# Kernel optimization log

Hardware: AMD Instinct MI355X
Metric: run time of the kernel (lower is better)

Reference implementation:

```python
import jax, jax.numpy as jnp
import numpy as np

EMB_DIM = 32
UID_TGT = 200000
IID_TGT = 50000
BATCH = 128
TOPK = 50000          # hardcoded inside test_source_free branch
TARGET_LABEL = 4.0    # module-level target rating constant


def setup_inputs() -> dict:
    key = jax.random.key(0)
    k1, k2, k3, k4, k5 = jax.random.split(key, 5)
    # x: column 0 = item id (stored as float, like the torch code), cols 1: = src_rate_pre
    iid = jax.random.randint(k1, (BATCH,), 0, IID_TGT).astype(jnp.float32)
    src_rate = jax.random.normal(k2, (BATCH, EMB_DIM), dtype=jnp.float32)
    x = jnp.concatenate([iid[:, None], src_rate], axis=1)  # [B, 1+D]
    uid_weight = 0.1 * jax.random.normal(k3, (UID_TGT, EMB_DIM), dtype=jnp.float32)
    iid_weight = 0.1 * jax.random.normal(k4, (IID_TGT, EMB_DIM), dtype=jnp.float32)
    rp_weight = 0.1 * jax.random.normal(k5, (EMB_DIM, EMB_DIM), dtype=jnp.float32)
    return {"x": x, "uid_weight": uid_weight, "iid_weight": iid_weight, "rp_weight": rp_weight}


def reference(x, uid_weight, iid_weight, rp_weight):
    # === stage == 'test_source_free' ===
    iid = x[:, 0].astype(jnp.int32)                     # [B]
    iid_emb = iid_weight[iid]                           # [B, D] item embedding gather
    src_rate_pre = x[:, 1:] @ rp_weight.T               # [B, D] Linear(emb,emb,bias=False)
    # |uid_emb . src_rate - target|  (torch: [U,B]; here kept [B,U])
    predict_rate = jnp.abs(src_rate_pre @ uid_weight.T - TARGET_LABEL)  # [B, U]
    # torch: full sort ascending + take first TOPK  ==  bottom-TOPK per row
    _, topk_idx = jax.lax.top_k(-predict_rate, TOPK)    # [B, TOPK]
    # voted rating = <selected user emb, item emb>; compute all dots once,
    # then gather (same math as gathering [B,TOPK,D] embeddings and dotting).
    all_scores = iid_emb @ uid_weight.T                 # [B, U]
    voted_rating = jnp.take_along_axis(all_scores, topk_idx, axis=1)  # [B, TOPK]
    mean_rating = jnp.mean(voted_rating, axis=1)        # [B]
    return mean_rating
```

## Files before the change

kernel.cpp:

```cpp
#include <hip/hip_runtime.h>
#include <hip/hip_bf16.h>
#include <stdint.h>

#define EMB    32
#define BATCH  128
#define NU     200000
#define KSEL   50000
#define XCOLS  33
#define SLOTS  32
#define G1     512
#define G2P    512
#define G2F    256
#define HISTW  (128 * 129)
#define T1     32
#define T2     64

#define OFF_SPRE   0
#define OFF_IIDE   16384
#define OFF_GHIST  32768
#define OFF_BASE16 163840
#define OFF_PREFIX 164352
#define OFF_M2     164864
#define OFF_EQ     165376
#define OFF_CAND   173568
#define OFF_PART   173568
#define PART_BYTES ((size_t)G1 * HISTW * 4)

__device__ __forceinline__ float xor1(float x) {
    int r = __builtin_amdgcn_update_dpp(0, __float_as_int(x), 0xB1, 0xF, 0xF, true);
    return __int_as_float(r);
}

__device__ __forceinline__ float dotrow(const float* __restrict__ c,
                                        const float* __restrict__ u) {
    float d = 0.f;
    #pragma unroll
    for (int q = 0; q < 8; ++q) {
        const float4 v = *(const float4*)(u + q * 4);
        d += c[4*q+0]*v.x + c[4*q+1]*v.y + c[4*q+2]*v.z + c[4*q+3]*v.w;
    }
    return d;
}

__global__ void prep_kernel(const float* __restrict__ x,
                            const float* __restrict__ iid_w,
                            const float* __restrict__ rp,
                            const float* __restrict__ uid,
                            float* __restrict__ s_pre,
                            float* __restrict__ iid_emb,
                            uint32_t* __restrict__ base16,
                            uint32_t* __restrict__ eq_cnt) {
    const int b = blockIdx.x;
    const int t = threadIdx.x;
    __shared__ float xr[EMB];
    if (t < EMB) xr[t] = x[b * XCOLS + 1 + t];
    if (t == 63) eq_cnt[b * 16] = 0u;
    __syncthreads();
    if (t < EMB) {
        float acc = 0.f;
        #pragma unroll
        for (int k = 0; k < EMB; ++k) acc += xr[k] * rp[t * EMB + k];
        s_pre[b * EMB + t] = acc;
    } else {
        const int d = t - EMB;
        const int iid = (int)x[b * XCOLS];
        iid_emb[b * EMB + d] = iid_w[(size_t)iid * EMB + d];
    }
    __syncthreads();
    if (t == 0) {
        float dot = 0.f;
        #pragma unroll
        for (int k = 0; k < EMB; ++k) dot += s_pre[b * EMB + k] * uid[k];
        const uint32_t bits = __float_as_uint(fabsf(dot - 4.0f));
        const uint32_t hi = bits >> 16;
        base16[b] = (hi > 128u) ? (hi - 128u) : 0u;
    }
}

__global__ void zero_kernel(uint32_t* __restrict__ p, int n) {
    int i = blockIdx.x * blockDim.x + threadIdx.x;
    if (i < n) p[i] = 0u;
}

template <bool PART>
__global__ __launch_bounds__(1024)
void sweep1_kernel(const float* __restrict__ s_pre,
                   const float* __restrict__ uid,
                   const uint32_t* __restrict__ base16,
                   uint32_t* __restrict__ gout,
                   int jchunk) {
    extern __shared__ uint32_t smem1[];
    uint32_t* hist = smem1;
    float* tiles = (float*)(smem1 + HISTW);
    const int t  = threadIdx.x;
    const int b  = t & 127;
    const int jl = t >> 7;
    for (int i = t; i < HISTW; i += 1024) hist[i] = 0u;
    float s[EMB];
    #pragma unroll
    for (int d = 0; d < EMB; ++d) s[d] = s_pre[b * EMB + d];
    const uint32_t base = base16[b];

    const int j0 = blockIdx.x * jchunk;
    const int jend = min(j0 + jchunk, NU);
    const int nt = (jend - j0 + T1 - 1) / T1;
    const int srow = t >> 5;

    {
        float v = 0.f;
        if (j0 + srow < NU) v = uid[(size_t)j0 * EMB + t];
        tiles[t] = v;
    }
    __syncthreads();

    for (int tt = 0; tt < nt; ++tt) {
        const int jt = j0 + tt * T1;
        const bool has_next = (tt + 1 < nt);
        float vnext = 0.f;
        if (has_next) {
            const int jn = jt + T1;
            if (jn + srow < NU) vnext = uid[(size_t)jn * EMB + t];
        }
        const float* tp = tiles + (tt & 1) * (T1 * EMB);
        const int lim = min(T1, jend - jt);
        for (int r = jl; r < lim; r += 8) {
            const float d0 = dotrow(s, tp + r * EMB);
            const uint32_t bits0 = __float_as_uint(fabsf(d0 - 4.0f));
            int dg0 = (int)(bits0 >> 16) - (int)base;
            dg0 = dg0 < 0 ? 0 : (dg0 > 255 ? 255 : dg0);
            atomicAdd(&hist[b * 129 + (dg0 >> 1)], 1u << ((dg0 & 1) * 16));
        }
        if (has_next) {
            tiles[((tt + 1) & 1) * (T1 * EMB) + t] = vnext;
        }
        __syncthreads();
    }
    if (PART) {
        uint32_t* part = gout + (size_t)blockIdx.x * HISTW;
        for (int i = t; i < HISTW; i += 1024) part[i] = hist[i];
    } else {
        for (int i = t; i < 128 * 256; i += 1024) {
            const int r = i >> 8, d = i & 255;
            const uint32_t c = (hist[r * 129 + (d >> 1)] >> ((d & 1) * 16)) & 0xFFFFu;
            if (c) atomicAdd(&gout[i], c);
        }
    }
}

__global__ void scan1_kernel(const uint32_t* __restrict__ ghist,
                             const uint32_t* __restrict__ base16,
                             uint32_t* __restrict__ prefix16,
                             uint32_t* __restrict__ m2) {
    const int b = threadIdx.x;
    uint32_t cum = 0, before = 0;
    int c1 = 255;
    for (int d = 0; d < 256; ++d) {
        const uint32_t c = ghist[b * 256 + d];
        if (cum + c >= (uint32_t)KSEL) { c1 = d; before = cum; break; }
        cum += c;
        if (d == 255) before = cum;
    }
    prefix16[b] = base16[b] + (uint32_t)c1;
    m2[b] = (uint32_t)KSEL - before;
}

__global__ __launch_bounds__(256)
void scan1_part_kernel(const uint32_t* __restrict__ part,
                       const uint32_t* __restrict__ base16,
                       uint32_t* __restrict__ prefix16,
                       uint32_t* __restrict__ m2) {
    const int row = blockIdx.x;
    const int t = threadIdx.x;
    __shared__ uint32_t h[256];
    const int sh = (t & 1) * 16;
    const uint32_t* p = part + (size_t)row * 129 + (t >> 1);
    uint32_t a0 = 0, a1 = 0, a2 = 0, a3 = 0;
    for (int g = 0; g < G1; g += 4) {
        a0 += (p[(size_t)(g + 0) * HISTW] >> sh) & 0xFFFFu;
        a1 += (p[(size_t)(g + 1) * HISTW] >> sh) & 0xFFFFu;
        a2 += (p[(size_t)(g + 2) * HISTW] >> sh) & 0xFFFFu;
        a3 += (p[(size_t)(g + 3) * HISTW] >> sh) & 0xFFFFu;
    }
    h[t] = a0 + a1 + a2 + a3;
    __syncthreads();
    if (t == 0) {
        uint32_t cum = 0, before = 0; int c1 = 255;
        for (int d = 0; d < 256; ++d) {
            const uint32_t c = h[d];
            if (cum + c >= (uint32_t)KSEL) { c1 = d; before = cum; break; }
            cum += c;
            if (d == 255) before = cum;
        }
        prefix16[row] = base16[row] + (uint32_t)c1;
        m2[row] = (uint32_t)KSEL - before;
    }
}

__global__ __launch_bounds__(1024)
void sweep2_kernel(const float* __restrict__ s_pre,
                   const float* __restrict__ iid_emb,
                   const float* __restrict__ uid,
                   const uint32_t* __restrict__ prefix16,
                   uint32_t* __restrict__ eq_cnt,
                   float* __restrict__ sum_part,
                   uint64_t* __restrict__ cand,
                   int cap, int jchunk) {
    extern __shared__ char smem2[];
    uint64_t* lcand  = (uint64_t*)smem2;
    float*    tiles  = (float*)(smem2 + 32768);
    uint32_t* lcnt   = (uint32_t*)(smem2 + 49152);
    uint32_t* lbase  = (uint32_t*)(smem2 + 49664);
    float*    sums_b = (float*)(smem2 + 50176);
    const int t   = threadIdx.x;
    const int par = t & 1;
    const int pr  = t >> 1;
    const int b   = pr & 127;
    const int jl  = pr >> 7;
    if (t < 128) { lcnt[t] = 0u; sums_b[t] = 0.f; }
    float c[EMB];
    {
        const float4* cp4 = (const float4*)((par ? iid_emb : s_pre) + b * EMB);
        #pragma unroll
        for (int q = 0; q < 8; ++q) {
            float4 v = cp4[q];
            c[4*q+0] = v.x; c[4*q+1] = v.y; c[4*q+2] = v.z; c[4*q+3] = v.w;
        }
    }
    const uint32_t pfx = prefix16[b];

    const int j0 = blockIdx.x * jchunk;
    const int jend = min(j0 + jchunk, NU);
    const int nt = (jend - j0 + T2 - 1) / T2;
    const int srow = t >> 4;

    {
        float2 v = make_float2(0.f, 0.f);
        if (j0 + srow < NU) v = *(const float2*)(uid + (size_t)j0 * EMB + t * 2);
        *(float2*)(tiles + t * 2) = v;
    }
    __syncthreads();

    float local = 0.f;
    for (int tt = 0; tt < nt; ++tt) {
        const int jt = j0 + tt * T2;
        const bool has_next = (tt + 1 < nt);
        float2 vnext = make_float2(0.f, 0.f);
        if (has_next) {
            const int jn = jt + T2;
            if (jn + srow < NU) vnext = *(const float2*)(uid + (size_t)jn * EMB + t * 2);
        }
        const float* tp = tiles + (tt & 1) * (T2 * EMB);
        const int lim = min(T2, jend - jt);
        for (int r = jl; r < lim; r += 4) {
            const float a0 = dotrow(c, tp + r * EMB);
            const float p0 = xor1(a0);
            if (par == 0) {
                const uint32_t bits0 = __float_as_uint(fabsf(a0 - 4.0f));
                const uint32_t hi0 = bits0 >> 16;
                local += (hi0 < pfx) ? p0 : 0.f;
                if (hi0 == pfx) {
                    const uint32_t pos = atomicAdd(&lcnt[b], 1u);
                    const uint64_t pk = ((uint64_t)bits0 << 32) | (uint32_t)(jt + r);
                    if (pos < (uint32_t)SLOTS) lcand[b * SLOTS + pos] = pk;
                    else {
                        const uint32_t g = atomicAdd(&eq_cnt[b * 16], 1u);
                        if (g < (uint32_t)cap) cand[(size_t)b * cap + g] = pk;
                    }
                }
            }
        }
        if (has_next) {
            *(float2*)(tiles + ((tt + 1) & 1) * (T2 * EMB) + t * 2) = vnext;
        }
        __syncthreads();
    }
    if (par == 0 && local != 0.f) atomicAdd(&sums_b[b], local);
    __syncthreads();
    if (t < 128) {
        sum_part[(size_t)blockIdx.x * 128 + t] = sums_b[t];
        const uint32_t n = min(lcnt[t], (uint32_t)SLOTS);
        lbase[t] = atomicAdd(&eq_cnt[t * 16], n);
    }
    __syncthreads();
    for (int i = t; i < 128 * SLOTS; i += 1024) {
        const int bb = i >> 5;
        const int sl = i & 31;
        if (sl < (int)min(lcnt[bb], (uint32_t)SLOTS)) {
            const uint32_t p = lbase[bb] + (uint32_t)sl;
            if (p < (uint32_t)cap) cand[(size_t)bb * cap + p] = lcand[i];
        }
    }
}

__global__ __launch_bounds__(256)
void final_kernel(const float* __restrict__ iid_emb,
                  const float* __restrict__ uid,
                  const uint32_t* __restrict__ m2_,
                  const uint32_t* __restrict__ eq_cnt,
                  const float* __restrict__ sum_part,
                  const uint64_t* __restrict__ cand,
                  int cap, int g2, float* __restrict__ out) {
    const int b = blockIdx.x;
    const int t = threadIdx.x;
    __shared__ float red[256];
    __shared__ uint32_t hist[256];
    __shared__ float e[EMB];
    __shared__ uint32_t tie[128];
    __shared__ uint32_t tiecnt, sc2, sm3, sc3, sm4;
    __shared__ float sbelow;
    if (t < EMB) e[t] = iid_emb[b * EMB + t];
    if (t == 0) tiecnt = 0u;
    hist[t] = 0u;
    {
        float acc = 0.f;
        for (int g = t; g < g2; g += 256) acc += sum_part[(size_t)g * 128 + b];
        red[t] = acc;
    }
    __syncthreads();
    for (int s = 128; s > 0; s >>= 1) { if (t < s) red[t] += red[t + s]; __syncthreads(); }
    if (t == 0) sbelow = red[0];
    __syncthreads();

    const uint32_t ec = eq_cnt[b * 16];
    const int cnt = (int)(ec < (uint32_t)cap ? ec : (uint32_t)cap);
    const uint64_t* cb = cand + (size_t)b * cap;

    for (int i = t; i < cnt; i += 256) {
        const uint32_t low16 = (uint32_t)(cb[i] >> 32) & 0xFFFFu;
        atomicAdd(&hist[low16 >> 8], 1u);
    }
    __syncthreads();
    if (t == 0) {
        const uint32_t m2v = m2_[b];
        uint32_t cum = 0, before = 0; int c2 = 255;
        for (int d = 0; d < 256; ++d) {
            const uint32_t c = hist[d];
            if (cum + c >= m2v) { c2 = d; before = cum; break; }
            cum += c;
        }
        sc2 = (uint32_t)c2; sm3 = m2v - before;
    }
    __syncthreads();
    const uint32_t c2 = sc2;
    hist[t] = 0u;
    __syncthreads();

    for (int i = t; i < cnt; i += 256) {
        const uint32_t low16 = (uint32_t)(cb[i] >> 32) & 0xFFFFu;
        if ((low16 >> 8) == c2) atomicAdd(&hist[low16 & 255u], 1u);
    }
    __syncthreads();
    if (t == 0) {
        const uint32_t m3 = sm3;
        uint32_t cum = 0, before = 0; int c3 = 255;
        for (int d = 0; d < 256; ++d) {
            const uint32_t c = hist[d];
            if (cum + c >= m3) { c3 = d; before = cum; break; }
            cum += c;
        }
        sc3 = (uint32_t)c3; sm4 = m3 - before;
    }
    __syncthreads();
    const uint32_t T16 = (c2 << 8) | sc3;

    float local = 0.f;
    for (int i = t; i < cnt; i += 256) {
        const uint64_t cv = cb[i];
        const uint32_t low16 = (uint32_t)(cv >> 32) & 0xFFFFu;
        if (low16 < T16) {
            const uint32_t j = (uint32_t)cv;
            const float4* u4 = (const float4*)(uid + (size_t)j * EMB);
            float dv = 0.f;
            #pragma unroll
            for (int q = 0; q < 8; ++q) {
                float4 u = u4[q];
                dv += e[4*q+0]*u.x + e[4*q+1]*u.y + e[4*q+2]*u.z + e[4*q+3]*u.w;
            }
            local += dv;
        } else if (low16 == T16) {
            const uint32_t pos = atomicAdd(&tiecnt, 1u);
            if (pos < 128u) tie[pos] = (uint32_t)cv;
        }
    }
    red[t] = local;
    __syncthreads();
    for (int s = 128; s > 0; s >>= 1) { if (t < s) red[t] += red[t + s]; __syncthreads(); }
    if (t == 0) {
        int tc = (int)(tiecnt < 128u ? tiecnt : 128u);
        for (int i = 1; i < tc; ++i) {
            const uint32_t v = tie[i]; int k = i - 1;
            while (k >= 0 && tie[k] > v) { tie[k+1] = tie[k]; --k; }
            tie[k+1] = v;
        }
        const int m4 = (int)sm4;
        float tsum = 0.f;
        for (int i = 0; i < m4 && i < tc; ++i) {
            const uint32_t j = tie[i];
            float dv = 0.f;
            for (int d = 0; d < EMB; ++d) dv += e[d] * uid[(size_t)j * EMB + d];
            tsum += dv;
        }
        out[b] = (sbelow + red[0] + tsum) / (float)KSEL;
    }
}

extern "C" void kernel_launch(void* const* d_in, const int* in_sizes, int n_in,
                              void* d_out, int out_size, void* d_ws, size_t ws_size,
                              hipStream_t stream) {
    const float* x     = (const float*)d_in[0];
    const float* uid   = (const float*)d_in[1];
    const float* iid_w = (const float*)d_in[2];
    const float* rp    = (const float*)d_in[3];
    float* out = (float*)d_out;

    char* ws = (char*)d_ws;
    float*    s_pre    = (float*)(ws + OFF_SPRE);
    float*    iid_emb  = (float*)(ws + OFF_IIDE);
    uint32_t* ghist    = (uint32_t*)(ws + OFF_GHIST);
    uint32_t* base16   = (uint32_t*)(ws + OFF_BASE16);
    uint32_t* prefix16 = (uint32_t*)(ws + OFF_PREFIX);
    uint32_t* m2       = (uint32_t*)(ws + OFF_M2);
    uint32_t* eq_cnt   = (uint32_t*)(ws + OFF_EQ);
    uint32_t* part     = (uint32_t*)(ws + OFF_PART);

    const size_t off_cand2 = OFF_PART + PART_BYTES;
    const bool use_part = ws_size >= off_cand2 + (size_t)128 * 8 * 4096;

    uint64_t* cand;
    int cap;
    float* sum_part;
    int g2;
    if (use_part) {
        cand = (uint64_t*)(ws + off_cand2);
        long long cap_ll = ((long long)ws_size - (long long)off_cand2) / (128LL * 8LL);
        cap = (int)(cap_ll > 16384 ? 16384 : cap_ll);
        sum_part = (float*)part;
        g2 = G2P;
    } else {
        cand = (uint64_t*)(ws + OFF_CAND);
        long long cap_ll = ((long long)ws_size - OFF_CAND) / (128LL * 8LL);
        cap = (int)(cap_ll > 16384 ? 16384 : (cap_ll < 1 ? 1 : cap_ll));
        sum_part = (float*)(ws + OFF_GHIST);
        g2 = G2F;
        const int n = (OFF_CAND - OFF_GHIST) / 4;
        zero_kernel<<<(n + 255) / 256, 256, 0, stream>>>((uint32_t*)(ws + OFF_GHIST), n);
    }

    prep_kernel<<<BATCH, 64, 0, stream>>>(x, iid_w, rp, uid, s_pre, iid_emb, base16, eq_cnt);

    const int jc1 = (NU + G1 - 1) / G1;
    const size_t lds1 = HISTW * 4 + 2 * T1 * EMB * 4;
    if (use_part) {
        sweep1_kernel<true><<<G1, 1024, lds1, stream>>>(s_pre, uid, base16, part, jc1);
        scan1_part_kernel<<<BATCH, 256, 0, stream>>>(part, base16, prefix16, m2);
    } else {
        sweep1_kernel<false><<<G1, 1024, lds1, stream>>>(s_pre, uid, base16, ghist, jc1);
        scan1_kernel<<<1, 128, 0, stream>>>(ghist, base16, prefix16, m2);
    }

    const int jc2 = (NU + g2 - 1) / g2;
    const size_t lds2 = 32768 + 16384 + 1536;
    sweep2_kernel<<<g2, 1024, lds2, stream>>>(s_pre, iid_emb, uid,
                                              prefix16, eq_cnt, sum_part,
                                              cand, cap, jc2);

    final_kernel<<<BATCH, 256, 0, stream>>>(iid_emb, uid, m2, eq_cnt, sum_part,
                                            cand, cap, g2, out);
}
```

Before: 225.3 us.

## Cache per-user high-16-bit digits in sweep1 to skip predict dot in sweep2

When the workspace is large enough, sweep1 now writes the high 16 bits of each |s·u-4| value to a [NU,128] uint16 buffer. A new sweep2 kernel reads these digits instead of recomputing the predict-rate dot product, so it computes only the item-score dot per user. Tie candidates store only the user index, and final_kernel recomputes their full bits. This trades about 51MB of extra global writes and reads against half of sweep2's arithmetic. The new path only runs if the workspace exceeds that size.

```diff
diff --git a/kernel.cpp b/kernel.cpp
--- a/kernel.cpp
+++ b/kernel.cpp
@@ -1,5 +1,4 @@
 #include <hip/hip_runtime.h>
-#include <hip/hip_bf16.h>
 #include <stdint.h>
 
 #define EMB    32
@@ -8,7 +7,9 @@
 #define KSEL   50000
 #define XCOLS  33
 #define SLOTS  32
+#define DSLOTS 16
 #define G1     512
+#define G2D    512
 #define G2P    512
 #define G2F    256
 #define HISTW  (128 * 129)
@@ -22,9 +23,11 @@
 #define OFF_PREFIX 164352
 #define OFF_M2     164864
 #define OFF_EQ     165376
-#define OFF_CAND   173568
-#define OFF_PART   173568
+#define OFF_BIG    173568
 #define PART_BYTES ((size_t)G1 * HISTW * 4)
+#define DIG_BYTES  ((size_t)NU * 128 * 2)
+#define OFF_PARTD  ((size_t)OFF_BIG + DIG_BYTES)
+#define OFF_CANDD  (OFF_PARTD + PART_BYTES)
 
 __device__ __forceinline__ float xor1(float x) {
     int r = __builtin_amdgcn_update_dpp(0, __float_as_int(x), 0xB1, 0xF, 0xF, true);
@@ -82,12 +85,13 @@
     if (i < n) p[i] = 0u;
 }
 
-template <bool PART>
+template <bool PART, bool DIG>
 __global__ __launch_bounds__(1024)
 void sweep1_kernel(const float* __restrict__ s_pre,
                    const float* __restrict__ uid,
                    const uint32_t* __restrict__ base16,
                    uint32_t* __restrict__ gout,
+                   uint16_t* __restrict__ dig,
                    int jchunk) {
     extern __shared__ uint32_t smem1[];
     uint32_t* hist = smem1;
@@ -126,7 +130,9 @@
         for (int r = jl; r < lim; r += 8) {
             const float d0 = dotrow(s, tp + r * EMB);
             const uint32_t bits0 = __float_as_uint(fabsf(d0 - 4.0f));
-            int dg0 = (int)(bits0 >> 16) - (int)base;
+            const uint32_t hi = bits0 >> 16;
+            if (DIG) dig[(size_t)(jt + r) * 128 + b] = (uint16_t)hi;
+            int dg0 = (int)hi - (int)base;
             dg0 = dg0 < 0 ? 0 : (dg0 > 255 ? 255 : dg0);
             atomicAdd(&hist[b * 129 + (dg0 >> 1)], 1u << ((dg0 & 1) * 16));
         }
@@ -197,14 +203,106 @@
 }
 
 __global__ __launch_bounds__(1024)
-void sweep2_kernel(const float* __restrict__ s_pre,
-                   const float* __restrict__ iid_emb,
-                   const float* __restrict__ uid,
-                   const uint32_t* __restrict__ prefix16,
-                   uint32_t* __restrict__ eq_cnt,
-                   float* __restrict__ sum_part,
-                   uint64_t* __restrict__ cand,
-                   int cap, int jchunk) {
+void sweep2_dig_kernel(const float* __restrict__ iid_emb,
+                       const float* __restrict__ uid,
+                       const uint16_t* __restrict__ dig,
+                       const uint32_t* __restrict__ prefix16,
+                       uint32_t* __restrict__ eq_cnt,
+                       float* __restrict__ sum_part,
+                       uint64_t* __restrict__ cand,
+                       int cap, int jchunk) {
+    __shared__ uint32_t lcand[128 * DSLOTS];
+    __shared__ float tiles[2][T2 * EMB];
+    __shared__ uint32_t lcnt[128];
+    __shared__ uint32_t lbase[128];
+    __shared__ float sums[1024];
+    const int t  = threadIdx.x;
+    const int b  = t & 127;
+    const int jl = t >> 7;
+    if (t < 128) lcnt[t] = 0u;
+    float e[EMB];
+    {
+        const float4* ep4 = (const float4*)(iid_emb + b * EMB);
+        #pragma unroll
+        for (int q = 0; q < 8; ++q) {
+            float4 v = ep4[q];
+            e[4*q+0]=v.x; e[4*q+1]=v.y; e[4*q+2]=v.z; e[4*q+3]=v.w;
+        }
+    }
+    const int pfx = (int)prefix16[b];
+
+    const int j0 = blockIdx.x * jchunk;
+    const int jend = min(j0 + jchunk, NU);
+    const int nt = (jend - j0 + T2 - 1) / T2;
+    const int srow = t >> 4;
+
+    {
+        float2 v = make_float2(0.f, 0.f);
+        if (j0 + srow < NU) v = *(const float2*)(uid + (size_t)j0 * EMB + t * 2);
+        *(float2*)(&tiles[0][0] + t * 2) = v;
+    }
+    __syncthreads();
+
+    float local = 0.f;
+    for (int tt = 0; tt < nt; ++tt) {
+        const int jt = j0 + tt * T2;
+        const bool has_next = (tt + 1 < nt);
+        float2 vnext = make_float2(0.f, 0.f);
+        if (has_next) {
+            const int jn = jt + T2;
+            if (jn + srow < NU) vnext = *(const float2*)(uid + (size_t)jn * EMB + t * 2);
+        }
+        const float* tp = &tiles[tt & 1][0];
+        const int lim = min(T2, jend - jt);
+        for (int r = jl; r < lim; r += 8) {
+            const int hi = (int)dig[(size_t)(jt + r) * 128 + b];
+            const float dv = dotrow(e, tp + r * EMB);
+            local += (hi < pfx) ? dv : 0.f;
+            if (hi == pfx) {
+                const uint32_t pos = atomicAdd(&lcnt[b], 1u);
+                const uint32_t jj = (uint32_t)(jt + r);
+                if (pos < (uint32_t)DSLOTS) lcand[b * DSLOTS + pos] = jj;
+                else {
+                    const uint32_t g = atomicAdd(&eq_cnt[b * 16], 1u);
+                    if (g < (uint32_t)cap) cand[(size_t)b * cap + g] = (uint64_t)jj;
+                }
+            }
+        }
+        if (has_next) {
+            *(float2*)(&tiles[(tt + 1) & 1][0] + t * 2) = vnext;
+        }
+        __syncthreads();
+    }
+    sums[t] = local;
+    __syncthreads();
+    if (t < 128) {
+        float acc = 0.f;
+        #pragma unroll
+        for (int l = 0; l < 8; ++l) acc += sums[l * 128 + t];
+        sum_part[(size_t)blockIdx.x * 128 + t] = acc;
+        const uint32_t n = min(lcnt[t], (uint32_t)DSLOTS);
+        lbase[t] = atomicAdd(&eq_cnt[t * 16], n);
+    }
+    __syncthreads();
+    for (int i = t; i < 128 * DSLOTS; i += 1024) {
+        const int bb = i >> 4;
+        const int sl = i & 15;
+        if (sl < (int)min(lcnt[bb], (uint32_t)DSLOTS)) {
+            const uint32_t p = lbase[bb] + (uint32_t)sl;
+            if (p < (uint32_t)cap) cand[(size_t)bb * cap + p] = (uint64_t)lcand[i];
+        }
+    }
+}
+
+__global__ __launch_bounds__(1024)
+void sweep2_fb_kernel(const float* __restrict__ s_pre,
+                      const float* __restrict__ iid_emb,
+                      const float* __restrict__ uid,
+                      const uint32_t* __restrict__ prefix16,
+                      uint32_t* __restrict__ eq_cnt,
+                      float* __restrict__ sum_part,
+                      uint64_t* __restrict__ cand,
+                      int cap, int jchunk) {
     extern __shared__ char smem2[];
     uint64_t* lcand  = (uint64_t*)smem2;
     float*    tiles  = (float*)(smem2 + 32768);
@@ -294,21 +392,24 @@
 
 __global__ __launch_bounds__(256)
 void final_kernel(const float* __restrict__ iid_emb,
+                  const float* __restrict__ s_pre,
                   const float* __restrict__ uid,
                   const uint32_t* __restrict__ m2_,
                   const uint32_t* __restrict__ eq_cnt,
                   const float* __restrict__ sum_part,
-                  const uint64_t* __restrict__ cand,
-                  int cap, int g2, float* __restrict__ out) {
+                  uint64_t* __restrict__ cand,
+                  int cap, int g2, int recompute,
+                  float* __restrict__ out) {
     const int b = blockIdx.x;
     const int t = threadIdx.x;
     __shared__ float red[256];
     __shared__ uint32_t hist[256];
     __shared__ float e[EMB];
+    __shared__ float sarr[EMB];
     __shared__ uint32_t tie[128];
     __shared__ uint32_t tiecnt, sc2, sm3, sc3, sm4;
     __shared__ float sbelow;
-    if (t < EMB) e[t] = iid_emb[b * EMB + t];
+    if (t < EMB) { e[t] = iid_emb[b * EMB + t]; sarr[t] = s_pre[b * EMB + t]; }
     if (t == 0) tiecnt = 0u;
     hist[t] = 0u;
     {
@@ -323,7 +424,17 @@
 
     const uint32_t ec = eq_cnt[b * 16];
     const int cnt = (int)(ec < (uint32_t)cap ? ec : (uint32_t)cap);
-    const uint64_t* cb = cand + (size_t)b * cap;
+    uint64_t* cb = cand + (size_t)b * cap;
+
+    if (recompute) {
+        for (int i = t; i < cnt; i += 256) {
+            const uint32_t j = (uint32_t)cb[i];
+            const float d = dotrow(sarr, uid + (size_t)j * EMB);
+            const uint32_t bits = __float_as_uint(fabsf(d - 4.0f));
+            cb[i] = ((uint64_t)bits << 32) | j;
+        }
+        __syncthreads();
+    }
 
     for (int i = t; i < cnt; i += 256) {
         const uint32_t low16 = (uint32_t)(cb[i] >> 32) & 0xFFFFu;
@@ -421,49 +532,68 @@
     uint32_t* prefix16 = (uint32_t*)(ws + OFF_PREFIX);
     uint32_t* m2       = (uint32_t*)(ws + OFF_M2);
     uint32_t* eq_cnt   = (uint32_t*)(ws + OFF_EQ);
-    uint32_t* part     = (uint32_t*)(ws + OFF_PART);
-
-    const size_t off_cand2 = OFF_PART + PART_BYTES;
-    const bool use_part = ws_size >= off_cand2 + (size_t)128 * 8 * 4096;
-
-    uint64_t* cand;
-    int cap;
-    float* sum_part;
-    int g2;
-    if (use_part) {
-        cand = (uint64_t*)(ws + off_cand2);
-        long long cap_ll = ((long long)ws_size - (long long)off_cand2) / (128LL * 8LL);
-        cap = (int)(cap_ll > 16384 ? 16384 : cap_ll);
-        sum_part = (float*)part;
-        g2 = G2P;
-    } else {
-        cand = (uint64_t*)(ws + OFF_CAND);
-        long long cap_ll = ((long long)ws_size - OFF_CAND) / (128LL * 8LL);
-        cap = (int)(cap_ll > 16384 ? 16384 : (cap_ll < 1 ? 1 : cap_ll));
-        sum_part = (float*)(ws + OFF_GHIST);
-        g2 = G2F;
-        const int n = (OFF_CAND - OFF_GHIST) / 4;
-        zero_kernel<<<(n + 255) / 256, 256, 0, stream>>>((uint32_t*)(ws + OFF_GHIST), n);
-    }
+
+    const bool use_dig  = ws_size >= OFF_CANDD + (size_t)128 * 2048 * 8;
+    const bool use_part = !use_dig &&
+                          ws_size >= (size_t)OFF_BIG + PART_BYTES + (size_t)128 * 8 * 4096;
 
     prep_kernel<<<BATCH, 64, 0, stream>>>(x, iid_w, rp, uid, s_pre, iid_emb, base16, eq_cnt);
 
     const int jc1 = (NU + G1 - 1) / G1;
     const size_t lds1 = HISTW * 4 + 2 * T1 * EMB * 4;
-    if (use_part) {
-        sweep1_kernel<true><<<G1, 1024, lds1, stream>>>(s_pre, uid, base16, part, jc1);
+
+    if (use_dig) {
+        uint16_t* dig      = (uint16_t*)(ws + OFF_BIG);
+        uint32_t* part     = (uint32_t*)(ws + OFF_PARTD);
+        float*    sum_part = (float*)(ws + OFF_PARTD);
+        uint64_t* cand     = (uint64_t*)(ws + OFF_CANDD);
+        long long cap_ll = ((long long)ws_size - (long long)OFF_CANDD) / (128LL * 8LL);
+        int cap = (int)(cap_ll > 16384 ? 16384 : cap_ll);
+
+        sweep1_kernel<true, true><<<G1, 1024, lds1, stream>>>(s_pre, uid, base16, part, dig, jc1);
         scan1_part_kernel<<<BATCH, 256, 0, stream>>>(part, base16, prefix16, m2);
+
+        const int jc2 = (NU + G2D - 1) / G2D;
+        sweep2_dig_kernel<<<G2D, 1024, 0, stream>>>(iid_emb, uid, dig, prefix16,
+                                                    eq_cnt, sum_part, cand, cap, jc2);
+
+        final_kernel<<<BATCH, 256, 0, stream>>>(iid_emb, s_pre, uid, m2, eq_cnt, sum_part,
+                                                cand, cap, G2D, 1, out);
+    } else if (use_part) {
+        uint32_t* part     = (uint32_t*)(ws + OFF_BIG);
+        float*    sum_part = (float*)(ws + OFF_BIG);
+        uint64_t* cand     = (uint64_t*)(ws + OFF_BIG + PART_BYTES);
+        long long cap_ll = ((long long)ws_size - (long long)(OFF_BIG + PART_BYTES)) / (128LL * 8LL);
+        int cap = (int)(cap_ll > 16384 ? 16384 : cap_ll);
+
+        sweep1_kernel<true, false><<<G1, 1024, lds1, stream>>>(s_pre, uid, base16, part, nullptr, jc1);
+        scan1_part_kernel<<<BATCH, 256, 0, stream>>>(part, base16, prefix16, m2);
+
+        const int jc2 = (NU + G2P - 1) / G2P;
+        const size_t lds2 = 32768 + 16384 + 1536;
+        sweep2_fb_kernel<<<G2P, 1024, lds2, stream>>>(s_pre, iid_emb, uid, prefix16,
+                                                      eq_cnt, sum_part, cand, cap, jc2);
+
+        final_kernel<<<BATCH, 256, 0, stream>>>(iid_emb, s_pre, uid, m2, eq_cnt, sum_part,
+                                                cand, cap, G2P, 0, out);
     } else {
-        sweep1_kernel<false><<<G1, 1024, lds1, stream>>>(s_pre, uid, base16, ghist, jc1);
+        uint64_t* cand     = (uint64_t*)(ws + OFF_BIG);
+        float*    sum_part = (float*)(ws + OFF_GHIST);
+        long long cap_ll = ((long long)ws_size - OFF_BIG) / (128LL * 8LL);
+        int cap = (int)(cap_ll > 16384 ? 16384 : (cap_ll < 1 ? 1 : cap_ll));
+
+        const int n = (OFF_BIG - OFF_GHIST) / 4;
+        zero_kernel<<<(n + 255) / 256, 256, 0, stream>>>((uint32_t*)(ws + OFF_GHIST), n);
+
+        sweep1_kernel<false, false><<<G1, 1024, lds1, stream>>>(s_pre, uid, base16, ghist, nullptr, jc1);
         scan1_kernel<<<1, 128, 0, stream>>>(ghist, base16, prefix16, m2);
-    }
-
-    const int jc2 = (NU + g2 - 1) / g2;
-    const size_t lds2 = 32768 + 16384 + 1536;
-    sweep2_kernel<<<g2, 1024, lds2, stream>>>(s_pre, iid_emb, uid,
-                                              prefix16, eq_cnt, sum_part,
-                                              cand, cap, jc2);
-
-    final_kernel<<<BATCH, 256, 0, stream>>>(iid_emb, uid, m2, eq_cnt, sum_part,
-                                            cand, cap, g2, out);
-}
+
+        const int jc2 = (NU + G2F - 1) / G2F;
+        const size_t lds2 = 32768 + 16384 + 1536;
+        sweep2_fb_kernel<<<G2F, 1024, lds2, stream>>>(s_pre, iid_emb, uid, prefix16,
+                                                      eq_cnt, sum_part, cand, cap, jc2);
+
+        final_kernel<<<BATCH, 256, 0, stream>>>(iid_emb, s_pre, uid, m2, eq_cnt, sum_part,
+                                                cand, cap, G2F, 0, out);
+    }
+}
```

Result: slower. 280.0 us (+24.3%).
